# Kernel tuning notes

Hardware: AMD Instinct MI355X
Metric: run time of the kernel (lower is better)

The kernel has to match this reference:

```python
import jax, jax.numpy as jnp
import numpy as np

EPSILON = float(np.finfo(np.float32).eps)  # torch finfo(float32).eps
EPS = 1e-05  # MvdrBeamformer eps


def setup_inputs() -> dict:
    key = jax.random.key(0)
    ks = jax.random.split(key, 5)
    N, C, F, T = 8, 8, 257, 1000
    ATT = 512
    return {
        "mask_s": jax.random.uniform(ks[0], (N, T, F), jnp.float32),
        "x_re": jax.random.normal(ks[1], (N, C, F, T), jnp.float32),
        "x_im": jax.random.normal(ks[2], (N, C, F, T), jnp.float32),
        "proj_w": jax.random.normal(ks[3], (ATT, F), jnp.float32) * 0.02,
        "proj_b": jnp.zeros((ATT,), jnp.float32),
        "gvec_w": jax.random.normal(ks[4], (1, ATT), jnp.float32) * 0.02,
        "gvec_b": jnp.zeros((1,), jnp.float32),
    }


def _estimate_covar(mask, spec):
    # mask: N x F x T (real), spec: N x F x C x T (complex) -> N x F x C x C
    nom = jnp.einsum('nfit,nfjt->nfij', spec * mask[:, :, None, :], spec.conj())
    den = jnp.maximum(mask.sum(-1), EPSILON)[..., None, None]
    return nom / den


def reference(mask_s, x_re, x_im, proj_w, proj_b, gvec_w, gvec_b):
    x = x_re + 1j * x_im  # N x C x F x T complex
    # mask normalization: inf-norm over time dim (dim=1 of N x T x F)
    max_abs = jnp.max(jnp.abs(mask_s), axis=1, keepdims=True)
    m = mask_s / (max_abs + EPSILON)
    m = m.transpose(0, 2, 1)            # N x F x T
    spec = x.transpose(0, 2, 1, 3)      # N x F x C x T
    Rs = _estimate_covar(m, spec)       # N x F x C x C
    Rn = _estimate_covar(1.0 - m, spec)
    C = Rs.shape[-1]
    eye_b = jnp.eye(C, dtype=bool)
    # ChannelAttention: zero diagonal, average off-diagonal per row
    Rs_od = jnp.where(eye_b, 0.0, Rs).sum(-1) / (C - 1)   # N x F x C complex
    feat = jnp.abs(Rs_od).transpose(0, 2, 1)              # N x C x F real
    proj = jnp.tanh(feat @ proj_w.T + proj_b)             # N x C x ATT
    g = (proj @ gvec_w.T + gvec_b)[..., 0]                # N x C
    u = jax.nn.softmax(g, axis=-1)                        # N x C real
    # MVDR weight derivation
    Rn_l = Rn + jnp.eye(C, dtype=Rn.dtype) * EPS
    Rn_inv = jnp.linalg.inv(Rn_l)                         # batched small complex inverse
    RiRs = jnp.einsum('nfij,nfjk->nfik', Rn_inv, Rs)
    tr = jnp.trace(RiRs, axis1=-2, axis2=-1) + EPS        # N x F complex
    w = jnp.einsum('nfic,nc->nfi', RiRs, u.astype(RiRs.dtype)) / tr[..., None]  # N x F x C
    w = w.transpose(0, 2, 1)                              # N x C x F
    beam = (w[..., None].conj() * x).sum(axis=1)          # N x F x T
    beam = beam.transpose(0, 2, 1)                        # N x T x F complex
    # return real/imag stacked so output is a real array
    return jnp.stack([beam.real, beam.imag], axis=-1)     # N x T x F x 2
```

## Files before the change

kernel.cpp:

```cpp
#include <hip/hip_runtime.h>
#include <math.h>

#define N_ 8
#define C_ 8
#define F_ 257
#define T_ 1000
#define ATT_ 512
#define NF_ (N_*F_)
#define TSPLIT_ 4
#define EPSILON_ 1.1920928955078125e-07f
#define EPS_ 1e-5f

__device__ inline float2 cmul(float2 a, float2 b){
  return make_float2(a.x*b.x - a.y*b.y, a.x*b.y + a.y*b.x);
}
__device__ inline float2 crecip(float2 a){
  float id = 1.0f/(a.x*a.x + a.y*a.y);
  return make_float2(a.x*id, -a.y*id);
}
__device__ inline float2 cdivz(float2 a, float2 b){
  float id = 1.0f/(b.x*b.x + b.y*b.y);
  return make_float2((a.x*b.x + a.y*b.y)*id, (a.y*b.x - a.x*b.y)*id);
}
__device__ inline float2 shfl2(float2 v, int src){
  return make_float2(__shfl(v.x, src, 64), __shfl(v.y, src, 64));
}

__global__ __launch_bounds__(256) void k1a_stats(
    const float* __restrict__ mask, float* __restrict__ maxv, float* __restrict__ summ)
{
  __shared__ float smx[8][33];
  __shared__ float ssm[8][33];
  const int n = blockIdx.y;
  const int f0 = blockIdx.x*32;
  const int tx = threadIdx.x, ty = threadIdx.y;
  const int f = f0 + tx;
  float mx = 0.f, sm = 0.f;
  if (f < F_){
    for (int t = ty; t < T_; t += 8){
      float v = mask[((size_t)n*T_ + t)*F_ + f];
      mx = fmaxf(mx, fabsf(v));
      sm += v;
    }
  }
  smx[ty][tx] = mx; ssm[ty][tx] = sm;
  __syncthreads();
  if (ty == 0 && f < F_){
    #pragma unroll
    for (int k=1;k<8;++k){ mx = fmaxf(mx, smx[k][tx]); sm += ssm[k][tx]; }
    maxv[n*F_ + f] = mx;
    summ[n*F_ + f] = sm/(mx + EPSILON_);
  }
}

__global__ __launch_bounds__(256) void k1b_transpose(
    const float* __restrict__ mask, const float* __restrict__ maxv, float* __restrict__ m_t)
{
  __shared__ float tile[32][33];
  const int n = blockIdx.z;
  const int f0 = blockIdx.y*32;
  const int t0 = blockIdx.x*32;
  const int tx = threadIdx.x, ty = threadIdx.y;
  const int f = f0 + tx;
  float inv = 0.f;
  if (f < F_) inv = 1.0f/(maxv[n*F_ + f] + EPSILON_);
  #pragma unroll
  for (int k=0;k<4;++k){
    const int tl = ty + 8*k;
    const int t = t0 + tl;
    float v = 0.f;
    if (f < F_ && t < T_) v = mask[((size_t)n*T_ + t)*F_ + f];
    tile[tl][tx] = v*inv;
  }
  __syncthreads();
  #pragma unroll
  for (int k=0;k<4;++k){
    const int fl = ty + 8*k;
    const int f2 = f0 + fl, t2 = t0 + tx;
    if (f2 < F_ && t2 < T_) m_t[((size_t)n*F_ + f2)*T_ + t2] = tile[tx][fl];
  }
}

__global__ __launch_bounds__(64, 2) void k2_covar(
    const float* __restrict__ xre, const float* __restrict__ xim,
    const float* __restrict__ m_t, float* __restrict__ part)
{
  const int nf = blockIdx.x;
  const int tc = blockIdx.y;
  const int n = nf / F_;
  const int f = nf % F_;
  const int lane = threadIdx.x;
  const int tbase = tc*256;
  const int nt = (tc == 3) ? (T_ - 768) : 256;
  const int tq = lane*4;
  const bool act = tq < nt;

  float xr[8][4], xi[8][4], mm[4];
  if (act){
    const float4 m4 = *(const float4*)(m_t + (size_t)nf*T_ + tbase + tq);
    mm[0]=m4.x; mm[1]=m4.y; mm[2]=m4.z; mm[3]=m4.w;
    #pragma unroll
    for (int c=0;c<8;++c){
      const size_t base = (((size_t)n*C_ + c)*F_ + f)*T_ + tbase + tq;
      const float4 r4 = *(const float4*)(xre + base);
      const float4 i4 = *(const float4*)(xim + base);
      xr[c][0]=r4.x; xr[c][1]=r4.y; xr[c][2]=r4.z; xr[c][3]=r4.w;
      xi[c][0]=i4.x; xi[c][1]=i4.y; xi[c][2]=i4.z; xi[c][3]=i4.w;
    }
  } else {
    mm[0]=mm[1]=mm[2]=mm[3]=0.f;
    #pragma unroll
    for (int c=0;c<8;++c){
      #pragma unroll
      for (int q=0;q<4;++q){ xr[c][q]=0.f; xi[c][q]=0.f; }
    }
  }

  float v[128];
  #pragma unroll
  for (int e=0;e<128;++e) v[e] = 0.f;

  #pragma unroll
  for (int q=0;q<4;++q){
    const float m = mm[q];
    #pragma unroll
    for (int d=0;d<8;++d){
      const float p = xr[d][q]*xr[d][q] + xi[d][q]*xi[d][q];
      v[2*d]   += p;
      v[2*d+1] += m*p;
    }
    #pragma unroll
    for (int a=0;a<8;++a){
      #pragma unroll
      for (int b=a+1;b<8;++b){
        const int e = 16 + 4*(a*(13-a)/2 + b - 1);
        const float pr = xr[a][q]*xr[b][q] + xi[a][q]*xi[b][q];
        const float pi = xi[a][q]*xr[b][q] - xr[a][q]*xi[b][q];
        v[e]   += pr;   v[e+1] += pi;
        v[e+2] += m*pr; v[e+3] += m*pi;
      }
    }
  }

  #define RSTEP(S, CNT, OFF) \
    _Pragma("unroll") \
    for (int k=0;k<CNT;++k){ \
      const float a_ = v[OFF+2*k], b_ = v[OFF+2*k+1]; \
      const bool hi = (lane & S) != 0; \
      const float mine = hi ? b_ : a_; \
      const float oth  = hi ? a_ : b_; \
      v[OFF+k] = mine + __shfl_xor(oth, S, 64); \
    }
  RSTEP(1,32,0) RSTEP(2,16,0) RSTEP(4,8,0) RSTEP(8,4,0) RSTEP(16,2,0) RSTEP(32,1,0)
  RSTEP(1,32,64) RSTEP(2,16,64) RSTEP(4,8,64) RSTEP(8,4,64) RSTEP(16,2,64) RSTEP(32,1,64)
  #undef RSTEP

  float* pp = part + ((size_t)tc*NF_ + nf)*128;
  pp[lane]      = v[0];
  pp[64 + lane] = v[64];
}

__global__ __launch_bounds__(64) void k2r_reduce(
    const float* __restrict__ part, const float* __restrict__ summ,
    float2* __restrict__ Rs, float2* __restrict__ Rn)
{
  const int nf = blockIdx.x;
  const int lane = threadIdx.x;
  const int i = lane >> 3, j = lane & 7;
  const int a = (i < j) ? i : j;
  const int b = (i < j) ? j : i;
  const float sgn = (i <= j) ? 1.f : -1.f;
  const int eo = 16 + 4*(a*(13-a)/2 + b - 1);
  float tr=0.f, ti=0.f, sr=0.f, si=0.f;
  #pragma unroll
  for (int tc=0; tc<TSPLIT_; ++tc){
    const float* p = part + ((size_t)tc*NF_ + nf)*128;
    if (i == j){
      tr += p[2*i];
      sr += p[2*i+1];
    } else {
      tr += p[eo];
      ti += sgn*p[eo+1];
      sr += p[eo+2];
      si += sgn*p[eo+3];
    }
  }
  const float sm = summ[nf];
  const float ids = 1.0f/fmaxf(sm, EPSILON_);
  const float idn = 1.0f/fmaxf((float)T_ - sm, EPSILON_);
  Rs[(size_t)nf*64 + lane] = make_float2(sr*ids, si*ids);
  Rn[(size_t)nf*64 + lane] = make_float2((tr-sr)*idn + ((i==j)?EPS_:0.f), (ti-si)*idn);
}

__global__ __launch_bounds__(256) void k3a_feat(
    const float2* __restrict__ Rs, float* __restrict__ feat)
{
  const int nc = blockIdx.x;
  const int n = nc >> 3, c = nc & 7;
  const int tid = threadIdx.x;
  for (int f = tid; f < F_; f += 256){
    const float2* row = Rs + (((size_t)n*F_ + f)*8 + c)*8;
    float sr = 0.f, si = 0.f;
    #pragma unroll
    for (int j=0;j<8;++j){ float2 v = row[j]; sr += v.x; si += v.y; }
    float2 d = row[c];
    sr = (sr - d.x)*(1.0f/7.0f);
    si = (si - d.y)*(1.0f/7.0f);
    feat[(size_t)nc*F_ + f] = sqrtf(sr*sr + si*si);
  }
}

__global__ __launch_bounds__(256) void k3b_proj(
    const float* __restrict__ feat, const float* __restrict__ proj_w,
    const float* __restrict__ proj_b, const float* __restrict__ gvec_w,
    float* __restrict__ partial3)
{
  const int nc = blockIdx.y;
  const int tid = threadIdx.x;
  const int wave = tid >> 6, lane = tid & 63;
  const int a0 = blockIdx.x*16 + wave*4;
  float acc0 = 0.f, acc1 = 0.f, acc2 = 0.f, acc3 = 0.f;
  const float* fr = feat + (size_t)nc*F_;
  const float* w0 = proj_w + (size_t)(a0+0)*F_;
  const float* w1 = proj_w + (size_t)(a0+1)*F_;
  const float* w2 = proj_w + (size_t)(a0+2)*F_;
  const float* w3 = proj_w + (size_t)(a0+3)*F_;
  for (int fi = lane; fi < F_; fi += 64){
    const float fv = fr[fi];
    acc0 += fv*w0[fi];
    acc1 += fv*w1[fi];
    acc2 += fv*w2[fi];
    acc3 += fv*w3[fi];
  }
  #pragma unroll
  for (int s=1;s<64;s<<=1){
    acc0 += __shfl_xor(acc0, s, 64);
    acc1 += __shfl_xor(acc1, s, 64);
    acc2 += __shfl_xor(acc2, s, 64);
    acc3 += __shfl_xor(acc3, s, 64);
  }
  if (lane == 0){
    float v = tanhf(acc0 + proj_b[a0+0])*gvec_w[a0+0]
            + tanhf(acc1 + proj_b[a0+1])*gvec_w[a0+1]
            + tanhf(acc2 + proj_b[a0+2])*gvec_w[a0+2]
            + tanhf(acc3 + proj_b[a0+3])*gvec_w[a0+3];
    partial3[(size_t)(blockIdx.x*4 + wave)*64 + nc] = v;
  }
}

__global__ __launch_bounds__(64) void k3c_gsum(
    const float* __restrict__ partial3, float* __restrict__ g)
{
  const int lane = threadIdx.x;
  float s = 0.f;
  #pragma unroll
  for (int p=0;p<128;++p) s += partial3[(size_t)p*64 + lane];
  g[lane] = s;
}

__global__ __launch_bounds__(256) void k4_solve(
    const float2* __restrict__ Rs, const float2* __restrict__ Rn,
    const float* __restrict__ g, float2* __restrict__ w_ws)
{
  const int tid = threadIdx.x;
  const int wid = blockIdx.x*4 + (tid >> 6);
  const int lane = tid & 63;
  const int ii = lane >> 3, jj = lane & 7;
  const int n = wid / F_;
  float2 A = Rn[(size_t)wid*64 + lane];
  float2 R = Rs[(size_t)wid*64 + lane];
  float gv = g[n*C_ + jj];
  float mx = gv;
  #pragma unroll
  for (int s=1;s<8;s<<=1) mx = fmaxf(mx, __shfl_xor(mx, s, 64));
  float e = expf(gv - mx);
  float es = e;
  #pragma unroll
  for (int s=1;s<8;s<<=1) es += __shfl_xor(es, s, 64);
  const float u = e / es;
  #pragma unroll
  for (int k=0;k<8;++k){
    float2 piv    = shfl2(A, k*9);
    float2 oldAkj = shfl2(A, k*8 + jj);
    float2 dum    = shfl2(A, ii*8 + k);
    float2 pinv = crecip(piv);
    float2 newk = (jj==k) ? pinv : cmul(oldAkj, pinv);
    if (ii == k){
      A = newk;
    } else {
      float2 b = (jj==k) ? make_float2(0.f,0.f) : A;
      float2 t = cmul(newk, dum);
      A = make_float2(b.x - t.x, b.y - t.y);
    }
  }
  float2 v = make_float2(R.x*u, R.y*u);
  #pragma unroll
  for (int s=1;s<8;s<<=1){ v.x += __shfl_xor(v.x, s, 64); v.y += __shfl_xor(v.y, s, 64); }
  float2 Rt = shfl2(R, jj*8 + ii);
  float2 tp = cmul(A, Rt);
  #pragma unroll
  for (int s=1;s<64;s<<=1){ tp.x += __shfl_xor(tp.x, s, 64); tp.y += __shfl_xor(tp.y, s, 64); }
  tp.x += EPS_;
  float2 vj = shfl2(v, jj*8);
  float2 q = cmul(A, vj);
  #pragma unroll
  for (int s=1;s<8;s<<=1){ q.x += __shfl_xor(q.x, s, 64); q.y += __shfl_xor(q.y, s, 64); }
  float2 wv = cdivz(q, tp);
  if (jj == 0) w_ws[(size_t)wid*8 + ii] = wv;
}

__global__ __launch_bounds__(256) void k5_beam(
    const float* __restrict__ xre, const float* __restrict__ xim,
    const float2* __restrict__ w_ws, float* __restrict__ out)
{
  __shared__ float b_re[32][129];
  __shared__ float b_im[32][129];
  __shared__ float2 w_l[32][8];
  const int n = blockIdx.z;
  const int f0 = blockIdx.y*32;
  const int t0 = blockIdx.x*128;
  const int tid = threadIdx.x;
  {
    const int fl = tid >> 3, c = tid & 7;
    const int f = f0 + fl;
    w_l[fl][c] = (f < F_) ? w_ws[((size_t)n*F_ + f)*8 + c] : make_float2(0.f,0.f);
  }
  __syncthreads();
  const int tq = (tid & 31)*4;
  const int fg = tid >> 5;
  const int t = t0 + tq;
  const bool tok = (t + 3) < T_;
  #pragma unroll
  for (int fi=0; fi<4; ++fi){
    const int fl = fg + fi*8;
    const int f = f0 + fl;
    float4 ar = make_float4(0,0,0,0), ai = make_float4(0,0,0,0);
    if (f < F_ && tok){
      #pragma unroll
      for (int c=0;c<8;++c){
        const size_t base = (((size_t)n*C_ + c)*F_ + f)*T_ + t;
        const float4 xr = *(const float4*)(xre + base);
        const float4 xi = *(const float4*)(xim + base);
        const float2 wv = w_l[fl][c];
        ar.x += wv.x*xr.x + wv.y*xi.x;  ai.x += wv.x*xi.x - wv.y*xr.x;
        ar.y += wv.x*xr.y + wv.y*xi.y;  ai.y += wv.x*xi.y - wv.y*xr.y;
        ar.z += wv.x*xr.z + wv.y*xi.z;  ai.z += wv.x*xi.z - wv.y*xr.z;
        ar.w += wv.x*xr.w + wv.y*xi.w;  ai.w += wv.x*xi.w - wv.y*xr.w;
      }
    }
    b_re[fl][tq+0]=ar.x; b_re[fl][tq+1]=ar.y; b_re[fl][tq+2]=ar.z; b_re[fl][tq+3]=ar.w;
    b_im[fl][tq+0]=ai.x; b_im[fl][tq+1]=ai.y; b_im[fl][tq+2]=ai.z; b_im[fl][tq+3]=ai.w;
  }
  __syncthreads();
  const int fl2 = tid & 31;
  const int tp = tid >> 5;
  const int f2 = f0 + fl2;
  if (f2 < F_){
    #pragma unroll
    for (int k=0;k<16;++k){
      const int tl = tp + k*8;
      const int t2 = t0 + tl;
      if (t2 < T_){
        float2 v = make_float2(b_re[fl2][tl], b_im[fl2][tl]);
        *(float2*)(out + (((size_t)n*T_ + t2)*F_ + f2)*2) = v;
      }
    }
  }
}

extern "C" void kernel_launch(void* const* d_in, const int* in_sizes, int n_in,
                              void* d_out, int out_size, void* d_ws, size_t ws_size,
                              hipStream_t stream)
{
  const float* mask   = (const float*)d_in[0];
  const float* xre    = (const float*)d_in[1];
  const float* xim    = (const float*)d_in[2];
  const float* proj_w = (const float*)d_in[3];
  const float* proj_b = (const float*)d_in[4];
  const float* gvec_w = (const float*)d_in[5];
  const float* gvec_b = (const float*)d_in[6];
  (void)gvec_b;
  float* out = (float*)d_out;
  char* ws = (char*)d_ws;

  size_t o = 0;
  auto alloc = [&](size_t bytes){ size_t r = o; o += (bytes + 255) & ~(size_t)255; return r; };
  float*  m_t   = (float*) (ws + alloc((size_t)N_*F_*T_*4));
  float*  maxv  = (float*) (ws + alloc((size_t)N_*F_*4));
  float*  summ  = (float*) (ws + alloc((size_t)N_*F_*4));
  float2* Rs    = (float2*)(ws + alloc((size_t)NF_*64*8));
  float2* Rn    = (float2*)(ws + alloc((size_t)NF_*64*8));
  float*  part  = (float*) (ws + alloc((size_t)TSPLIT_*NF_*128*4));
  float*  g     = (float*) (ws + alloc((size_t)N_*C_*4));
  float*  feat  = (float*) (ws + alloc((size_t)N_*C_*F_*4));
  float*  part3 = (float*) (ws + alloc((size_t)128*64*4));
  float2* w_ws  = (float2*)(ws + alloc((size_t)NF_*C_*8));

  k1a_stats    <<<dim3(9, N_),        dim3(32,8), 0, stream>>>(mask, maxv, summ);
  k1b_transpose<<<dim3(32, 9, N_),    dim3(32,8), 0, stream>>>(mask, maxv, m_t);
  k2_covar     <<<dim3(NF_, TSPLIT_), dim3(64),   0, stream>>>(xre, xim, m_t, part);
  k2r_reduce   <<<dim3(NF_),          dim3(64),   0, stream>>>(part, summ, Rs, Rn);
  k3a_feat     <<<dim3(N_*C_),        dim3(256),  0, stream>>>(Rs, feat);
  k3b_proj     <<<dim3(32, N_*C_),    dim3(256),  0, stream>>>(feat, proj_w, proj_b, gvec_w, part3);
  k3c_gsum     <<<dim3(1),            dim3(64),   0, stream>>>(part3, g);
  k4_solve     <<<dim3(NF_/4),        dim3(256),  0, stream>>>(Rs, Rn, g, w_ws);
  k5_beam      <<<dim3(8, 9, N_),     dim3(256),  0, stream>>>(xre, xim, w_ws, out);
}
```

Baseline: 274.0 us.

## Fuse mask stats into transpose and defer max-normalization to covariance reduce

The separate stats kernel, which walked the whole mask with only 72 blocks, is merged into the transpose kernel. That kernel now writes the raw transposed mask plus per-chunk partial max and sum values. A small new kernel reduces those partials, and the 1/max scaling is applied once per (n,f) in the covariance reduction, since the covariance is linear in the mask. This removes one full pass over the mask and a poorly parallel kernel, at the cost of an extra launch and some partial-buffer traffic.

After: 235.0 us. 14.2% less time.

```diff
diff --git a/kernel.cpp b/kernel.cpp
--- a/kernel.cpp
+++ b/kernel.cpp
@@ -8,6 +8,7 @@
 #define ATT_ 512
 #define NF_ (N_*F_)
 #define TSPLIT_ 4
+#define TCHUNKS1_ 32
 #define EPSILON_ 1.1920928955078125e-07f
 #define EPS_ 1e-5f
 
@@ -26,64 +27,64 @@
   return make_float2(__shfl(v.x, src, 64), __shfl(v.y, src, 64));
 }
 
-__global__ __launch_bounds__(256) void k1a_stats(
-    const float* __restrict__ mask, float* __restrict__ maxv, float* __restrict__ summ)
-{
+__global__ __launch_bounds__(256) void k1_fused(
+    const float* __restrict__ mask, float* __restrict__ mask_t,
+    float* __restrict__ pmax, float* __restrict__ psum)
+{
+  __shared__ float tile[32][33];
   __shared__ float smx[8][33];
   __shared__ float ssm[8][33];
-  const int n = blockIdx.y;
-  const int f0 = blockIdx.x*32;
-  const int tx = threadIdx.x, ty = threadIdx.y;
-  const int f = f0 + tx;
-  float mx = 0.f, sm = 0.f;
-  if (f < F_){
-    for (int t = ty; t < T_; t += 8){
-      float v = mask[((size_t)n*T_ + t)*F_ + f];
-      mx = fmaxf(mx, fabsf(v));
-      sm += v;
-    }
-  }
-  smx[ty][tx] = mx; ssm[ty][tx] = sm;
-  __syncthreads();
-  if (ty == 0 && f < F_){
-    #pragma unroll
-    for (int k=1;k<8;++k){ mx = fmaxf(mx, smx[k][tx]); sm += ssm[k][tx]; }
-    maxv[n*F_ + f] = mx;
-    summ[n*F_ + f] = sm/(mx + EPSILON_);
-  }
-}
-
-__global__ __launch_bounds__(256) void k1b_transpose(
-    const float* __restrict__ mask, const float* __restrict__ maxv, float* __restrict__ m_t)
-{
-  __shared__ float tile[32][33];
   const int n = blockIdx.z;
   const int f0 = blockIdx.y*32;
   const int t0 = blockIdx.x*32;
   const int tx = threadIdx.x, ty = threadIdx.y;
   const int f = f0 + tx;
-  float inv = 0.f;
-  if (f < F_) inv = 1.0f/(maxv[n*F_ + f] + EPSILON_);
+  float mx = 0.f, sm = 0.f;
   #pragma unroll
   for (int k=0;k<4;++k){
     const int tl = ty + 8*k;
     const int t = t0 + tl;
     float v = 0.f;
     if (f < F_ && t < T_) v = mask[((size_t)n*T_ + t)*F_ + f];
-    tile[tl][tx] = v*inv;
-  }
+    tile[tl][tx] = v;
+    mx = fmaxf(mx, fabsf(v));
+    sm += v;
+  }
+  smx[ty][tx] = mx; ssm[ty][tx] = sm;
   __syncthreads();
   #pragma unroll
   for (int k=0;k<4;++k){
     const int fl = ty + 8*k;
     const int f2 = f0 + fl, t2 = t0 + tx;
-    if (f2 < F_ && t2 < T_) m_t[((size_t)n*F_ + f2)*T_ + t2] = tile[tx][fl];
-  }
+    if (f2 < F_ && t2 < T_) mask_t[((size_t)n*F_ + f2)*T_ + t2] = tile[tx][fl];
+  }
+  if (ty == 0 && f < F_){
+    #pragma unroll
+    for (int k=1;k<8;++k){ mx = fmaxf(mx, smx[k][tx]); sm += ssm[k][tx]; }
+    pmax[(size_t)blockIdx.x*NF_ + n*F_ + f] = mx;
+    psum[(size_t)blockIdx.x*NF_ + n*F_ + f] = sm;
+  }
+}
+
+__global__ __launch_bounds__(256) void k1r_reduce(
+    const float* __restrict__ pmax, const float* __restrict__ psum,
+    float* __restrict__ maxv, float* __restrict__ summ)
+{
+  const int idx = blockIdx.x*256 + threadIdx.x;
+  if (idx >= NF_) return;
+  float mx = 0.f, sm = 0.f;
+  #pragma unroll
+  for (int c=0;c<TCHUNKS1_;++c){
+    mx = fmaxf(mx, pmax[(size_t)c*NF_ + idx]);
+    sm += psum[(size_t)c*NF_ + idx];
+  }
+  maxv[idx] = mx;
+  summ[idx] = sm/(mx + EPSILON_);
 }
 
 __global__ __launch_bounds__(64, 2) void k2_covar(
     const float* __restrict__ xre, const float* __restrict__ xim,
-    const float* __restrict__ m_t, float* __restrict__ part)
+    const float* __restrict__ mask_t, float* __restrict__ part)
 {
   const int nf = blockIdx.x;
   const int tc = blockIdx.y;
@@ -97,7 +98,7 @@
 
   float xr[8][4], xi[8][4], mm[4];
   if (act){
-    const float4 m4 = *(const float4*)(m_t + (size_t)nf*T_ + tbase + tq);
+    const float4 m4 = *(const float4*)(mask_t + (size_t)nf*T_ + tbase + tq);
     mm[0]=m4.x; mm[1]=m4.y; mm[2]=m4.z; mm[3]=m4.w;
     #pragma unroll
     for (int c=0;c<8;++c){
@@ -161,7 +162,8 @@
 }
 
 __global__ __launch_bounds__(64) void k2r_reduce(
-    const float* __restrict__ part, const float* __restrict__ summ,
+    const float* __restrict__ part, const float* __restrict__ maxv,
+    const float* __restrict__ summ,
     float2* __restrict__ Rs, float2* __restrict__ Rn)
 {
   const int nf = blockIdx.x;
@@ -185,6 +187,8 @@
       si += sgn*p[eo+3];
     }
   }
+  const float inv = 1.0f/(maxv[nf] + EPSILON_);
+  sr *= inv; si *= inv;
   const float sm = summ[nf];
   const float ids = 1.0f/fmaxf(sm, EPSILON_);
   const float idn = 1.0f/fmaxf((float)T_ - sm, EPSILON_);
@@ -385,24 +389,26 @@
 
   size_t o = 0;
   auto alloc = [&](size_t bytes){ size_t r = o; o += (bytes + 255) & ~(size_t)255; return r; };
-  float*  m_t   = (float*) (ws + alloc((size_t)N_*F_*T_*4));
-  float*  maxv  = (float*) (ws + alloc((size_t)N_*F_*4));
-  float*  summ  = (float*) (ws + alloc((size_t)N_*F_*4));
-  float2* Rs    = (float2*)(ws + alloc((size_t)NF_*64*8));
-  float2* Rn    = (float2*)(ws + alloc((size_t)NF_*64*8));
-  float*  part  = (float*) (ws + alloc((size_t)TSPLIT_*NF_*128*4));
-  float*  g     = (float*) (ws + alloc((size_t)N_*C_*4));
-  float*  feat  = (float*) (ws + alloc((size_t)N_*C_*F_*4));
-  float*  part3 = (float*) (ws + alloc((size_t)128*64*4));
-  float2* w_ws  = (float2*)(ws + alloc((size_t)NF_*C_*8));
-
-  k1a_stats    <<<dim3(9, N_),        dim3(32,8), 0, stream>>>(mask, maxv, summ);
-  k1b_transpose<<<dim3(32, 9, N_),    dim3(32,8), 0, stream>>>(mask, maxv, m_t);
-  k2_covar     <<<dim3(NF_, TSPLIT_), dim3(64),   0, stream>>>(xre, xim, m_t, part);
-  k2r_reduce   <<<dim3(NF_),          dim3(64),   0, stream>>>(part, summ, Rs, Rn);
-  k3a_feat     <<<dim3(N_*C_),        dim3(256),  0, stream>>>(Rs, feat);
-  k3b_proj     <<<dim3(32, N_*C_),    dim3(256),  0, stream>>>(feat, proj_w, proj_b, gvec_w, part3);
-  k3c_gsum     <<<dim3(1),            dim3(64),   0, stream>>>(part3, g);
-  k4_solve     <<<dim3(NF_/4),        dim3(256),  0, stream>>>(Rs, Rn, g, w_ws);
-  k5_beam      <<<dim3(8, 9, N_),     dim3(256),  0, stream>>>(xre, xim, w_ws, out);
-}
+  float*  mask_t = (float*) (ws + alloc((size_t)N_*F_*T_*4));
+  float*  maxv   = (float*) (ws + alloc((size_t)NF_*4));
+  float*  summ   = (float*) (ws + alloc((size_t)NF_*4));
+  float*  pmax   = (float*) (ws + alloc((size_t)TCHUNKS1_*NF_*4));
+  float*  psum   = (float*) (ws + alloc((size_t)TCHUNKS1_*NF_*4));
+  float2* Rs     = (float2*)(ws + alloc((size_t)NF_*64*8));
+  float2* Rn     = (float2*)(ws + alloc((size_t)NF_*64*8));
+  float*  part   = (float*) (ws + alloc((size_t)TSPLIT_*NF_*128*4));
+  float*  g      = (float*) (ws + alloc((size_t)N_*C_*4));
+  float*  feat   = (float*) (ws + alloc((size_t)N_*C_*F_*4));
+  float*  part3  = (float*) (ws + alloc((size_t)128*64*4));
+  float2* w_ws   = (float2*)(ws + alloc((size_t)NF_*C_*8));
+
+  k1_fused   <<<dim3(TCHUNKS1_, 9, N_), dim3(32,8), 0, stream>>>(mask, mask_t, pmax, psum);
+  k1r_reduce <<<dim3((NF_+255)/256),    dim3(256),  0, stream>>>(pmax, psum, maxv, summ);
+  k2_covar   <<<dim3(NF_, TSPLIT_),     dim3(64),   0, stream>>>(xre, xim, mask_t, part);
+  k2r_reduce <<<dim3(NF_),              dim3(64),   0, stream>>>(part, maxv, summ, Rs, Rn);
+  k3a_feat   <<<dim3(N_*C_),            dim3(256),  0, stream>>>(Rs, feat);
+  k3b_proj   <<<dim3(32, N_*C_),        dim3(256),  0, stream>>>(feat, proj_w, proj_b, gvec_w, part3);
+  k3c_gsum   <<<dim3(1),                dim3(64),   0, stream>>>(part3, g);
+  k4_solve   <<<dim3(NF_/4),            dim3(256),  0, stream>>>(Rs, Rn, g, w_ws);
+  k5_beam    <<<dim3(8, 9, N_),         dim3(256),  0, stream>>>(xre, xim, w_ws, out);
+}
```
